# Kernel optimization log

Measured on AMD Instinct MI355X. Metric: run time of the kernel, lower is better.

Reference implementation:

```python
import jax, jax.numpy as jnp
import numpy as np

B, N, F = 1024, 256, 8
E = 1024
OUT = 128          # NNConv out-channels (hardcoded in module)
N_DIV = 64         # len(num_actions)
PER = 3            # actions per diverter
FEAT = N * OUT     # feature_size() = num_nodes * 128


def setup_inputs() -> dict:
    key = jax.random.key(0)
    ks = jax.random.split(key, 20)
    s = lambda *sh: 0.02
    return {
        "x": jax.random.normal(ks[0], (B, N, F), jnp.float32),
        "edge_index": jax.random.randint(ks[1], (2, E), 0, N, jnp.int64),
        # edge-MLP nn1: Linear(1,64) -> ReLU -> Linear(64, F*OUT)
        "w1": jax.random.normal(ks[2], (1, 64), jnp.float32) * 0.1,
        "b1": jnp.zeros((64,), jnp.float32),
        "w2": jax.random.normal(ks[3], (64, F * OUT), jnp.float32) * 0.02,
        "b2": jnp.zeros((F * OUT,), jnp.float32),
        # NNConv root weight + bias
        "root_w": jax.random.normal(ks[4], (F, OUT), jnp.float32) * 0.1,
        "conv_b": jnp.zeros((OUT,), jnp.float32),
        # dueling heads
        "adv_w": jax.random.normal(ks[5], (FEAT, N_DIV * PER), jnp.float32) * 0.005,
        "adv_b": jnp.zeros((N_DIV * PER,), jnp.float32),
        "v1w": jax.random.normal(ks[6], (FEAT, 64), jnp.float32) * 0.005,
        "v1b": jnp.zeros((64,), jnp.float32),
        "v2w": jax.random.normal(ks[7], (64, 64), jnp.float32) * 0.1,
        "v2b": jnp.zeros((64,), jnp.float32),
        "v3w": jax.random.normal(ks[8], (64, N_DIV), jnp.float32) * 0.1,
        "v3b": jnp.zeros((N_DIV,), jnp.float32),
    }


def reference(x, edge_index, w1, b1, w2, b2, root_w, conv_b,
              adv_w, adv_b, v1w, v1b, v2w, v2b, v3w, v3b):
    b, n, f = x.shape
    out_c = root_w.shape[1]
    n_div = v3w.shape[1]
    flat = x.reshape(b * n, f)                              # [B*N, F]
    e = edge_index.shape[1]
    # edge_attr = ones -> edge MLP produces per-edge weight matrix theta
    ea = jnp.ones((e, 1), x.dtype)
    h = jax.nn.relu(ea @ w1 + b1)
    theta = (h @ w2 + b2).reshape(e, f, out_c)              # [E, F, OUT]
    src, tgt = edge_index[0], edge_index[1]
    # gather source feats -> per-edge matmul -> scatter-add at targets
    msg = jnp.einsum('ef,efo->eo', flat[src], theta)        # [E, OUT]
    agg = jnp.zeros((b * n, out_c), x.dtype).at[tgt].add(msg)
    conv = agg + flat @ root_w + conv_b                      # NNConv root + bias
    feat = jax.nn.relu(conv).reshape(b, -1)                  # [B, N*OUT]
    adv = jax.nn.relu(feat @ adv_w + adv_b).reshape(b, n_div, -1)
    val = jax.nn.relu(feat @ v1w + v1b)
    val = jax.nn.relu(val @ v2w + v2b)
    val = val @ v3w + v3b                                    # [B, n_div]
    return val[..., None] + adv - adv.mean(-1, keepdims=True)
```

## Files before the change

kernel.cpp:

```cpp
#include <hip/hip_runtime.h>

#define Bsz 1024
#define Nn 256
#define Fdim 8
#define Eedge 1024
#define OUTC 128
#define CADV 192
#define CTOT 256
#define Ktot 32768
#define ASTR 40
#define XSTR 24

typedef __attribute__((ext_vector_type(8))) short short8;
typedef __attribute__((ext_vector_type(4))) float float4v;

static __device__ inline unsigned short f2bf(float f) {
  union { float f; unsigned u; } v; v.f = f;
  unsigned r = v.u + 0x7FFFu + ((v.u >> 16) & 1u);
  return (unsigned short)(r >> 16);
}
static __device__ inline float bf2f(unsigned short h) {
  union { unsigned u; float f; } v; v.u = ((unsigned)h) << 16;
  return v.f;
}
static __device__ inline uint4 pack8(const unsigned short* b) {
  uint4 v;
  v.x = (unsigned)b[0] | ((unsigned)b[1] << 16);
  v.y = (unsigned)b[2] | ((unsigned)b[3] << 16);
  v.z = (unsigned)b[4] | ((unsigned)b[5] << 16);
  v.w = (unsigned)b[6] | ((unsigned)b[7] << 16);
  return v;
}

__global__ __launch_bounds__(256) void prep_feat_kernel(
    const float* __restrict__ x, const int* __restrict__ ei,
    const float* __restrict__ w1, const float* __restrict__ b1,
    const float* __restrict__ w2, const float* __restrict__ b2,
    const float* __restrict__ rootw, const float* __restrict__ convb,
    const float* __restrict__ advw, const float* __restrict__ v1w,
    unsigned short* __restrict__ wt, unsigned short* __restrict__ feat0)
{
  __shared__ __align__(16) char smem[20480];
  int bid = blockIdx.x, t = threadIdx.x;

  if (bid < 16) {
    float* fs   = (float*)smem;
    float* h_s  = fs;
    float* rw_s = fs + 64;
    float* th_s = fs + 128;
    float* pt_s = fs + 192;
    float* S_s  = fs + 448;
    int*   flag = (int*)(fs + 2496);
    int obase = bid * 8;

    if (t < 64) {
      h_s[t]  = fmaxf(w1[t] + b1[t], 0.f);
      rw_s[t] = rootw[(t >> 3) * OUTC + obase + (t & 7)];
    }
    for (int i = t; i < Nn * Fdim; i += 256) S_s[i] = 0.f;
    if (t == 0) {
      int z = 0;
      for (int i = 1; i < 16; i += 2) z |= ei[i];
      *flag = (z == 0);
    }
    __syncthreads();
    int is64 = *flag;

    {
      int l = t & 63, g = t >> 6;
      int c = (l >> 3) * 128 + obase + (l & 7);
      float p = 0.f;
#pragma unroll
      for (int j = 0; j < 16; ++j)
        p += h_s[g * 16 + j] * w2[(size_t)(g * 16 + j) * 1024 + c];
      pt_s[t] = p;
    }
    int srcs[4], tgts[4];
#pragma unroll
    for (int q = 0; q < 4; ++q) {
      int e = t + q * 256;
      if (is64) { srcs[q] = ei[2 * e]; tgts[q] = ei[2 * (Eedge + e)]; }
      else      { srcs[q] = ei[e];     tgts[q] = ei[Eedge + e]; }
      srcs[q] &= 255; tgts[q] &= 255;
    }
    __syncthreads();
    if (t < 64) {
      int c = (t >> 3) * 128 + obase + (t & 7);
      th_s[t] = b2[c] + pt_s[t] + pt_s[t + 64] + pt_s[t + 128] + pt_s[t + 192];
    }
#pragma unroll
    for (int q = 0; q < 4; ++q) {
      const float* xp = x + srcs[q] * Fdim;
#pragma unroll
      for (int f = 0; f < Fdim; ++f)
        atomicAdd(&S_s[tgts[q] * Fdim + f], xp[f]);
    }
    __syncthreads();
    {
      int n = t;
      const float* xp = x + n * Fdim;
      float4 xa = *(const float4*)xp;
      float4 xb = *(const float4*)(xp + 4);
      float xv[8] = {xa.x, xa.y, xa.z, xa.w, xb.x, xb.y, xb.z, xb.w};
      float sv[8];
#pragma unroll
      for (int f = 0; f < 8; ++f) sv[f] = S_s[n * Fdim + f];
      unsigned short buf[8];
#pragma unroll
      for (int oi = 0; oi < 8; ++oi) {
        float z = convb[obase + oi];
#pragma unroll
        for (int f = 0; f < 8; ++f)
          z += xv[f] * rw_s[f * 8 + oi] + sv[f] * th_s[f * 8 + oi];
        buf[oi] = f2bf(fmaxf(z, 0.f));
      }
      *(uint4*)(feat0 + (size_t)n * OUTC + obase) = pack8(buf);
    }
  } else {
    unsigned short* st = (unsigned short*)smem;
    int kt = bid - 16, c = t;
    const float* src; int stride, col;
    if (c < CADV) { src = advw; stride = CADV; col = c; }
    else          { src = v1w;  stride = 64;   col = c - CADV; }
    float v[32];
#pragma unroll
    for (int i = 0; i < 32; ++i)
      v[i] = src[(size_t)(kt * 32 + i) * stride + col];
    unsigned short bv[32];
#pragma unroll
    for (int i = 0; i < 32; ++i) bv[i] = f2bf(v[i]);
#pragma unroll
    for (int p = 0; p < 4; ++p)
      *(uint4*)(st + c * ASTR + p * 8) = pack8(bv + p * 8);
    __syncthreads();
    uint4* dst = (uint4*)(wt + (size_t)kt * (CTOT * 32));
    for (int r = 0; r < 4; ++r) {
      int w = r * 256 + c;
      int wn = w >> 8, j = (w >> 6) & 3, ln = w & 63;
      int c2 = wn * 64 + j * 16 + (ln & 15);
      int ks = ln >> 4;
      dst[w] = *(const uint4*)(st + c2 * ASTR + ks * 8);
    }
  }
}

__global__ __launch_bounds__(512, 2) void gemm_mfma(
    const float* __restrict__ x, const unsigned short* __restrict__ wt,
    const float* __restrict__ rootw, const float* __restrict__ convb,
    const unsigned short* __restrict__ feat0, float* __restrict__ part,
    int iters, int ns)
{
  __shared__ short a_s[2][128 * ASTR];
  __shared__ short x_s[2][128 * XSTR];
  __shared__ short rw_s[128 * XSTR];
  __shared__ float convb_s[128];
  int t = threadIdx.x;
  int ch = blockIdx.x;
  int mb = blockIdx.y;
  int wave = t >> 6, lane = t & 63;
  int wm = wave >> 2, wn = wave & 3;
  int lm = lane & 15, lq = lane >> 4;

  float4v acc[4][4];
#pragma unroll
  for (int i = 0; i < 4; ++i)
#pragma unroll
    for (int j = 0; j < 4; ++j) acc[i][j] = (float4v)0.f;

  int kt0 = ch * iters;
  int iters4 = iters >> 2;
  int n0 = ch * iters4;
  int boff = wn * 256 + lane;

  if (t < 128) {
    float wv[8];
#pragma unroll
    for (int f = 0; f < 8; ++f) wv[f] = rootw[f * OUTC + t];
    unsigned short wh[8], wl[8];
#pragma unroll
    for (int f = 0; f < 8; ++f) {
      wh[f] = f2bf(wv[f]);
      wl[f] = f2bf(wv[f] - bf2f(wh[f]));
    }
    *(uint4*)(rw_s + t * XSTR)     = pack8(wh);
    *(uint4*)(rw_s + t * XSTR + 8) = pack8(wl);
    convb_s[t] = convb[t];
  }
  int xr = (t & 255) >> 1, xh = t & 1;
  const float* xgb = x + ((size_t)(mb * 128 + xr) * Nn) * Fdim + xh * 4;
  if (t < 256) {
    float4 xv = *(const float4*)(xgb + (size_t)n0 * Fdim);
    float xa[4] = {xv.x, xv.y, xv.z, xv.w};
    unsigned short hh[4], ll[4];
#pragma unroll
    for (int f = 0; f < 4; ++f) {
      hh[f] = f2bf(xa[f]);
      ll[f] = f2bf(xa[f] - bf2f(hh[f]));
    }
    uint2 dh, dl;
    dh.x = (unsigned)hh[0] | ((unsigned)hh[1] << 16);
    dh.y = (unsigned)hh[2] | ((unsigned)hh[3] << 16);
    dl.x = (unsigned)ll[0] | ((unsigned)ll[1] << 16);
    dl.y = (unsigned)ll[2] | ((unsigned)ll[3] << 16);
    *(uint2*)(x_s[0] + xr * XSTR + xh * 4)     = dh;
    *(uint2*)(x_s[0] + xr * XSTR + 8 + xh * 4) = dl;
  }
  __syncthreads();

  {
    int bloc = wave * 16 + lm;
    short8 xf = (short8)0;
    if (lq == 0 || lq == 2) xf = *(const short8*)(x_s[0] + bloc * XSTR);
    else if (lq == 1)       xf = *(const short8*)(x_s[0] + bloc * XSTR + 8);
#pragma unroll
    for (int tt = 0; tt < 2; ++tt) {
      int ot = tt;
      short8 wf = (short8)0;
      if (lq <= 1)      wf = *(const short8*)(rw_s + (ot * 16 + lm) * XSTR);
      else if (lq == 2) wf = *(const short8*)(rw_s + (ot * 16 + lm) * XSTR + 8);
      float4v c = __builtin_amdgcn_mfma_f32_16x16x32_bf16(wf, xf, (float4v)0.f, 0, 0, 0);
      int o0 = ot * 16 + lq * 4;
      float4 cb = *(const float4*)(convb_s + o0);
      unsigned d0 = (unsigned)f2bf(fmaxf(c[0] + cb.x, 0.f)) |
                    ((unsigned)f2bf(fmaxf(c[1] + cb.y, 0.f)) << 16);
      unsigned d1 = (unsigned)f2bf(fmaxf(c[2] + cb.z, 0.f)) |
                    ((unsigned)f2bf(fmaxf(c[3] + cb.w, 0.f)) << 16);
      if (mb == 0 && bloc == 0) {
        const unsigned* f0p = (const unsigned*)(feat0 + ((size_t)n0 * OUTC + o0));
        d0 = f0p[0]; d1 = f0p[1];
      }
      uint2 dd; dd.x = d0; dd.y = d1;
      *(uint2*)(a_s[0] + bloc * ASTR + tt * 16 + lq * 4) = dd;
    }
  }

  const uint4* gB = (const uint4*)wt;
  uint4 vb0, vb1, vb2, vb3;
  {
    const uint4* gq = gB + (size_t)kt0 * 1024 + boff;
    vb0 = gq[0]; vb1 = gq[64]; vb2 = gq[128]; vb3 = gq[192];
  }
  float4 xpf = {0.f, 0.f, 0.f, 0.f};

  for (int kk = 0; kk < iters; ++kk) {
    int g = kk & 3, grp = kk >> 2;
    if (g == 3 && grp + 1 < iters4 && t < 256) {
      float xa[4] = {xpf.x, xpf.y, xpf.z, xpf.w};
      unsigned short hh[4], ll[4];
#pragma unroll
      for (int f = 0; f < 4; ++f) {
        hh[f] = f2bf(xa[f]);
        ll[f] = f2bf(xa[f] - bf2f(hh[f]));
      }
      uint2 dh, dl;
      dh.x = (unsigned)hh[0] | ((unsigned)hh[1] << 16);
      dh.y = (unsigned)hh[2] | ((unsigned)hh[3] << 16);
      dl.x = (unsigned)ll[0] | ((unsigned)ll[1] << 16);
      dl.y = (unsigned)ll[2] | ((unsigned)ll[3] << 16);
      short* xd = x_s[(grp + 1) & 1];
      *(uint2*)(xd + xr * XSTR + xh * 4)     = dh;
      *(uint2*)(xd + xr * XSTR + 8 + xh * 4) = dl;
    }
    __syncthreads();

    uint4 vbn0, vbn1, vbn2, vbn3;
    bool pf = (kk + 1 < iters);
    if (pf) {
      const uint4* gq = gB + (size_t)(kt0 + kk + 1) * 1024 + boff;
      vbn0 = gq[0]; vbn1 = gq[64]; vbn2 = gq[128]; vbn3 = gq[192];
    }
    if (g == 0 && grp + 1 < iters4 && t < 256)
      xpf = *(const float4*)(xgb + (size_t)(n0 + grp + 1) * Fdim);

    short* ab = a_s[kk & 1];
    short8 aF[4];
#pragma unroll
    for (int i = 0; i < 4; ++i)
      aF[i] = *(const short8*)(ab + (wm * 64 + i * 16 + lm) * ASTR + lq * 8);
    {
      short8 bF;
      bF = *(short8*)&vb0;
#pragma unroll
      for (int i = 0; i < 4; ++i)
        acc[i][0] = __builtin_amdgcn_mfma_f32_16x16x32_bf16(bF, aF[i], acc[i][0], 0, 0, 0);
      bF = *(short8*)&vb1;
#pragma unroll
      for (int i = 0; i < 4; ++i)
        acc[i][1] = __builtin_amdgcn_mfma_f32_16x16x32_bf16(bF, aF[i], acc[i][1], 0, 0, 0);
      bF = *(short8*)&vb2;
#pragma unroll
      for (int i = 0; i < 4; ++i)
        acc[i][2] = __builtin_amdgcn_mfma_f32_16x16x32_bf16(bF, aF[i], acc[i][2], 0, 0, 0);
      bF = *(short8*)&vb3;
#pragma unroll
      for (int i = 0; i < 4; ++i)
        acc[i][3] = __builtin_amdgcn_mfma_f32_16x16x32_bf16(bF, aF[i], acc[i][3], 0, 0, 0);
    }

    if (pf) {
      int kn = kk + 1;
      int g2 = kn & 3, grp2 = kn >> 2;
      const short* xs = x_s[grp2 & 1];
      int node2 = n0 + grp2;
      short* ad = a_s[kn & 1];
      int bloc = wave * 16 + lm;
      short8 xf = (short8)0;
      if (lq == 0 || lq == 2) xf = *(const short8*)(xs + bloc * XSTR);
      else if (lq == 1)       xf = *(const short8*)(xs + bloc * XSTR + 8);
#pragma unroll
      for (int tt = 0; tt < 2; ++tt) {
        int ot = g2 * 2 + tt;
        short8 wf = (short8)0;
        if (lq <= 1)      wf = *(const short8*)(rw_s + (ot * 16 + lm) * XSTR);
        else if (lq == 2) wf = *(const short8*)(rw_s + (ot * 16 + lm) * XSTR + 8);
        float4v c = __builtin_amdgcn_mfma_f32_16x16x32_bf16(wf, xf, (float4v)0.f, 0, 0, 0);
        int o0 = ot * 16 + lq * 4;
        float4 cb = *(const float4*)(convb_s + o0);
        unsigned d0 = (unsigned)f2bf(fmaxf(c[0] + cb.x, 0.f)) |
                      ((unsigned)f2bf(fmaxf(c[1] + cb.y, 0.f)) << 16);
        unsigned d1 = (unsigned)f2bf(fmaxf(c[2] + cb.z, 0.f)) |
                      ((unsigned)f2bf(fmaxf(c[3] + cb.w, 0.f)) << 16);
        if (mb == 0 && bloc == 0) {
          const unsigned* f0p = (const unsigned*)(feat0 + ((size_t)node2 * OUTC + o0));
          d0 = f0p[0]; d1 = f0p[1];
        }
        uint2 dd; dd.x = d0; dd.y = d1;
        *(uint2*)(ad + bloc * ASTR + tt * 16 + lq * 4) = dd;
      }
      vb0 = vbn0; vb1 = vbn1; vb2 = vbn2; vb3 = vbn3;
    }
  }

  float* pb = part + ((size_t)(mb * 128) * ns + ch) * CTOT;
#pragma unroll
  for (int i = 0; i < 4; ++i) {
    int m = wm * 64 + i * 16 + lm;
#pragma unroll
    for (int j = 0; j < 4; ++j) {
      int c = wn * 64 + j * 16 + lq * 4;
      *(float4v*)(pb + (size_t)m * ns * CTOT + c) = acc[i][j];
    }
  }
}

__global__ __launch_bounds__(256) void final_kernel(
    const float* __restrict__ part, int ns,
    const float* __restrict__ advb, const float* __restrict__ v1b,
    const float* __restrict__ v2w, const float* __restrict__ v2b,
    const float* __restrict__ v3w, const float* __restrict__ v3b,
    float* __restrict__ out)
{
  __shared__ float adv_s[CADV];
  __shared__ float v1_s[64];
  __shared__ float val2_s[64];
  __shared__ float val3_s[64];
  int b = blockIdx.x, t = threadIdx.x;
  float s = 0.f;
  const float* p = part + (size_t)b * ns * CTOT + t;
  for (int i = 0; i < ns; ++i) s += p[(size_t)i * CTOT];
  if (t < CADV) adv_s[t] = fmaxf(s + advb[t], 0.f);
  else          v1_s[t - CADV] = fmaxf(s + v1b[t - CADV], 0.f);
  __syncthreads();
  if (t < 64) {
    float a = v2b[t];
#pragma unroll
    for (int i = 0; i < 64; ++i) a += v1_s[i] * v2w[i * 64 + t];
    val2_s[t] = fmaxf(a, 0.f);
  }
  __syncthreads();
  if (t < 64) {
    float a = v3b[t];
#pragma unroll
    for (int j = 0; j < 64; ++j) a += val2_s[j] * v3w[j * 64 + t];
    val3_s[t] = a;
  }
  __syncthreads();
  if (t < CADV) {
    int d = t / 3;
    float mean = (adv_s[d * 3] + adv_s[d * 3 + 1] + adv_s[d * 3 + 2]) * (1.f / 3.f);
    out[(size_t)b * CADV + t] = val3_s[d] + adv_s[t] - mean;
  }
}

extern "C" void kernel_launch(void* const* d_in, const int* in_sizes, int n_in,
                              void* d_out, int out_size, void* d_ws, size_t ws_size,
                              hipStream_t stream)
{
  (void)in_sizes; (void)n_in; (void)out_size;
  const float* x     = (const float*)d_in[0];
  const int*   ei    = (const int*)d_in[1];
  const float* w1    = (const float*)d_in[2];
  const float* b1    = (const float*)d_in[3];
  const float* w2    = (const float*)d_in[4];
  const float* b2    = (const float*)d_in[5];
  const float* rootw = (const float*)d_in[6];
  const float* convb = (const float*)d_in[7];
  const float* advw  = (const float*)d_in[8];
  const float* advb  = (const float*)d_in[9];
  const float* v1w   = (const float*)d_in[10];
  const float* v1b   = (const float*)d_in[11];
  const float* v2w   = (const float*)d_in[12];
  const float* v2b   = (const float*)d_in[13];
  const float* v3w   = (const float*)d_in[14];
  const float* v3b   = (const float*)d_in[15];
  float* out = (float*)d_out;

  const size_t f0B = 131072;
  const size_t wtB = (size_t)Ktot * CTOT * 2;

  int NS = 64;
  while (NS > 8 && f0B + wtB + (size_t)NS * Bsz * CTOT * 4 > ws_size)
    NS >>= 1;

  unsigned short* feat0 = (unsigned short*)d_ws;
  unsigned short* wtp   = (unsigned short*)((char*)d_ws + f0B);
  float* part = (float*)((char*)d_ws + f0B + wtB);

  prep_feat_kernel<<<1040, 256, 0, stream>>>(x, ei, w1, b1, w2, b2, rootw,
                                             convb, advw, v1w, wtp, feat0);
  gemm_mfma<<<dim3(NS, 8), 512, 0, stream>>>(x, wtp, rootw, convb, feat0, part,
                                             1024 / NS, NS);
  final_kernel<<<Bsz, 256, 0, stream>>>(part, NS, advb, v1b, v2w, v2b, v3w, v3b, out);
}
```

Measured before the change: 185.5 us.

## Halve GEMM M-tile to 64 rows, double grid, drop B register prefetch

Shrinks the per-block batch tile in the MFMA GEMM from 128 to 64 rows, doubles the grid's M dimension to 16 and raises the launch-bounds occupancy hint from 2 to 4 blocks. Each wave now builds a single 16-column slice of the root-conv A tile instead of two. The one-iteration-ahead register prefetch of the weight fragments is removed, so B is loaded at the top of each iteration. The goal is more concurrent blocks and fewer registers to hide latency, at the price of reading the bf16 weight stream twice as many times and losing the explicit B prefetch.

```diff
diff --git a/kernel.cpp b/kernel.cpp
--- a/kernel.cpp
+++ b/kernel.cpp
@@ -144,14 +144,14 @@
   }
 }
 
-__global__ __launch_bounds__(512, 2) void gemm_mfma(
+__global__ __launch_bounds__(512, 4) void gemm_mfma(
     const float* __restrict__ x, const unsigned short* __restrict__ wt,
     const float* __restrict__ rootw, const float* __restrict__ convb,
     const unsigned short* __restrict__ feat0, float* __restrict__ part,
     int iters, int ns)
 {
-  __shared__ short a_s[2][128 * ASTR];
-  __shared__ short x_s[2][128 * XSTR];
+  __shared__ short a_s[2][64 * ASTR];
+  __shared__ short x_s[2][64 * XSTR];
   __shared__ short rw_s[128 * XSTR];
   __shared__ float convb_s[128];
   int t = threadIdx.x;
@@ -161,9 +161,9 @@
   int wm = wave >> 2, wn = wave & 3;
   int lm = lane & 15, lq = lane >> 4;
 
-  float4v acc[4][4];
-#pragma unroll
-  for (int i = 0; i < 4; ++i)
+  float4v acc[2][4];
+#pragma unroll
+  for (int i = 0; i < 2; ++i)
 #pragma unroll
     for (int j = 0; j < 4; ++j) acc[i][j] = (float4v)0.f;
 
@@ -171,6 +171,8 @@
   int iters4 = iters >> 2;
   int n0 = ch * iters4;
   int boff = wn * 256 + lane;
+  int bloc2 = (wave & 3) * 16 + lm;
+  int ttg = wave >> 2;
 
   if (t < 128) {
     float wv[8];
@@ -186,9 +188,9 @@
     *(uint4*)(rw_s + t * XSTR + 8) = pack8(wl);
     convb_s[t] = convb[t];
   }
-  int xr = (t & 255) >> 1, xh = t & 1;
-  const float* xgb = x + ((size_t)(mb * 128 + xr) * Nn) * Fdim + xh * 4;
-  if (t < 256) {
+  int xr = (t & 127) >> 1, xh = t & 1;
+  const float* xgb = x + ((size_t)(mb * 64 + xr) * Nn) * Fdim + xh * 4;
+  if (t < 128) {
     float4 xv = *(const float4*)(xgb + (size_t)n0 * Fdim);
     float xa[4] = {xv.x, xv.y, xv.z, xv.w};
     unsigned short hh[4], ll[4];
@@ -208,43 +210,34 @@
   __syncthreads();
 
   {
-    int bloc = wave * 16 + lm;
     short8 xf = (short8)0;
-    if (lq == 0 || lq == 2) xf = *(const short8*)(x_s[0] + bloc * XSTR);
-    else if (lq == 1)       xf = *(const short8*)(x_s[0] + bloc * XSTR + 8);
-#pragma unroll
-    for (int tt = 0; tt < 2; ++tt) {
-      int ot = tt;
-      short8 wf = (short8)0;
-      if (lq <= 1)      wf = *(const short8*)(rw_s + (ot * 16 + lm) * XSTR);
-      else if (lq == 2) wf = *(const short8*)(rw_s + (ot * 16 + lm) * XSTR + 8);
-      float4v c = __builtin_amdgcn_mfma_f32_16x16x32_bf16(wf, xf, (float4v)0.f, 0, 0, 0);
-      int o0 = ot * 16 + lq * 4;
-      float4 cb = *(const float4*)(convb_s + o0);
-      unsigned d0 = (unsigned)f2bf(fmaxf(c[0] + cb.x, 0.f)) |
-                    ((unsigned)f2bf(fmaxf(c[1] + cb.y, 0.f)) << 16);
-      unsigned d1 = (unsigned)f2bf(fmaxf(c[2] + cb.z, 0.f)) |
-                    ((unsigned)f2bf(fmaxf(c[3] + cb.w, 0.f)) << 16);
-      if (mb == 0 && bloc == 0) {
-        const unsigned* f0p = (const unsigned*)(feat0 + ((size_t)n0 * OUTC + o0));
-        d0 = f0p[0]; d1 = f0p[1];
-      }
-      uint2 dd; dd.x = d0; dd.y = d1;
-      *(uint2*)(a_s[0] + bloc * ASTR + tt * 16 + lq * 4) = dd;
-    }
+    if (lq == 0 || lq == 2) xf = *(const short8*)(x_s[0] + bloc2 * XSTR);
+    else if (lq == 1)       xf = *(const short8*)(x_s[0] + bloc2 * XSTR + 8);
+    int ot = ttg;
+    short8 wf = (short8)0;
+    if (lq <= 1)      wf = *(const short8*)(rw_s + (ot * 16 + lm) * XSTR);
+    else if (lq == 2) wf = *(const short8*)(rw_s + (ot * 16 + lm) * XSTR + 8);
+    float4v c = __builtin_amdgcn_mfma_f32_16x16x32_bf16(wf, xf, (float4v)0.f, 0, 0, 0);
+    int o0 = ot * 16 + lq * 4;
+    float4 cb = *(const float4*)(convb_s + o0);
+    unsigned d0 = (unsigned)f2bf(fmaxf(c[0] + cb.x, 0.f)) |
+                  ((unsigned)f2bf(fmaxf(c[1] + cb.y, 0.f)) << 16);
+    unsigned d1 = (unsigned)f2bf(fmaxf(c[2] + cb.z, 0.f)) |
+                  ((unsigned)f2bf(fmaxf(c[3] + cb.w, 0.f)) << 16);
+    if (mb == 0 && bloc2 == 0) {
+      const unsigned* f0p = (const unsigned*)(feat0 + ((size_t)n0 * OUTC + o0));
+      d0 = f0p[0]; d1 = f0p[1];
+    }
+    uint2 dd; dd.x = d0; dd.y = d1;
+    *(uint2*)(a_s[0] + bloc2 * ASTR + ttg * 16 + lq * 4) = dd;
   }
 
   const uint4* gB = (const uint4*)wt;
-  uint4 vb0, vb1, vb2, vb3;
-  {
-    const uint4* gq = gB + (size_t)kt0 * 1024 + boff;
-    vb0 = gq[0]; vb1 = gq[64]; vb2 = gq[128]; vb3 = gq[192];
-  }
   float4 xpf = {0.f, 0.f, 0.f, 0.f};
 
   for (int kk = 0; kk < iters; ++kk) {
     int g = kk & 3, grp = kk >> 2;
-    if (g == 3 && grp + 1 < iters4 && t < 256) {
+    if (g == 3 && grp + 1 < iters4 && t < 128) {
       float xa[4] = {xpf.x, xpf.y, xpf.z, xpf.w};
       unsigned short hh[4], ll[4];
 #pragma unroll
@@ -263,78 +256,69 @@
     }
     __syncthreads();
 
-    uint4 vbn0, vbn1, vbn2, vbn3;
-    bool pf = (kk + 1 < iters);
-    if (pf) {
-      const uint4* gq = gB + (size_t)(kt0 + kk + 1) * 1024 + boff;
-      vbn0 = gq[0]; vbn1 = gq[64]; vbn2 = gq[128]; vbn3 = gq[192];
-    }
-    if (g == 0 && grp + 1 < iters4 && t < 256)
+    const uint4* gq = gB + (size_t)(kt0 + kk) * 1024 + boff;
+    uint4 vb0 = gq[0], vb1 = gq[64], vb2 = gq[128], vb3 = gq[192];
+    if (g == 0 && grp + 1 < iters4 && t < 128)
       xpf = *(const float4*)(xgb + (size_t)(n0 + grp + 1) * Fdim);
 
     short* ab = a_s[kk & 1];
-    short8 aF[4];
-#pragma unroll
-    for (int i = 0; i < 4; ++i)
-      aF[i] = *(const short8*)(ab + (wm * 64 + i * 16 + lm) * ASTR + lq * 8);
+    short8 aF[2];
+#pragma unroll
+    for (int i = 0; i < 2; ++i)
+      aF[i] = *(const short8*)(ab + (wm * 32 + i * 16 + lm) * ASTR + lq * 8);
     {
       short8 bF;
       bF = *(short8*)&vb0;
 #pragma unroll
-      for (int i = 0; i < 4; ++i)
+      for (int i = 0; i < 2; ++i)
         acc[i][0] = __builtin_amdgcn_mfma_f32_16x16x32_bf16(bF, aF[i], acc[i][0], 0, 0, 0);
       bF = *(short8*)&vb1;
 #pragma unroll
-      for (int i = 0; i < 4; ++i)
+      for (int i = 0; i < 2; ++i)
         acc[i][1] = __builtin_amdgcn_mfma_f32_16x16x32_bf16(bF, aF[i], acc[i][1], 0, 0, 0);
       bF = *(short8*)&vb2;
 #pragma unroll
-      for (int i = 0; i < 4; ++i)
+      for (int i = 0; i < 2; ++i)
         acc[i][2] = __builtin_amdgcn_mfma_f32_16x16x32_bf16(bF, aF[i], acc[i][2], 0, 0, 0);
       bF = *(short8*)&vb3;
 #pragma unroll
-      for (int i = 0; i < 4; ++i)
+      for (int i = 0; i < 2; ++i)
         acc[i][3] = __builtin_amdgcn_mfma_f32_16x16x32_bf16(bF, aF[i], acc[i][3], 0, 0, 0);
     }
 
-    if (pf) {
+    if (kk + 1 < iters) {
       int kn = kk + 1;
       int g2 = kn & 3, grp2 = kn >> 2;
       const short* xs = x_s[grp2 & 1];
       int node2 = n0 + grp2;
       short* ad = a_s[kn & 1];
-      int bloc = wave * 16 + lm;
       short8 xf = (short8)0;
-      if (lq == 0 || lq == 2) xf = *(const short8*)(xs + bloc * XSTR);
-      else if (lq == 1)       xf = *(const short8*)(xs + bloc * XSTR + 8);
-#pragma unroll
-      for (int tt = 0; tt < 2; ++tt) {
-        int ot = g2 * 2 + tt;
-        short8 wf = (short8)0;
-        if (lq <= 1)      wf = *(const short8*)(rw_s + (ot * 16 + lm) * XSTR);
-        else if (lq == 2) wf = *(const short8*)(rw_s + (ot * 16 + lm) * XSTR + 8);
-        float4v c = __builtin_amdgcn_mfma_f32_16x16x32_bf16(wf, xf, (float4v)0.f, 0, 0, 0);
-        int o0 = ot * 16 + lq * 4;
-        float4 cb = *(const float4*)(convb_s + o0);
-        unsigned d0 = (unsigned)f2bf(fmaxf(c[0] + cb.x, 0.f)) |
-                      ((unsigned)f2bf(fmaxf(c[1] + cb.y, 0.f)) << 16);
-        unsigned d1 = (unsigned)f2bf(fmaxf(c[2] + cb.z, 0.f)) |
-                      ((unsigned)f2bf(fmaxf(c[3] + cb.w, 0.f)) << 16);
-        if (mb == 0 && bloc == 0) {
-          const unsigned* f0p = (const unsigned*)(feat0 + ((size_t)node2 * OUTC + o0));
-          d0 = f0p[0]; d1 = f0p[1];
-        }
-        uint2 dd; dd.x = d0; dd.y = d1;
-        *(uint2*)(ad + bloc * ASTR + tt * 16 + lq * 4) = dd;
+      if (lq == 0 || lq == 2) xf = *(const short8*)(xs + bloc2 * XSTR);
+      else if (lq == 1)       xf = *(const short8*)(xs + bloc2 * XSTR + 8);
+      int ot = g2 * 2 + ttg;
+      short8 wf = (short8)0;
+      if (lq <= 1)      wf = *(const short8*)(rw_s + (ot * 16 + lm) * XSTR);
+      else if (lq == 2) wf = *(const short8*)(rw_s + (ot * 16 + lm) * XSTR + 8);
+      float4v c = __builtin_amdgcn_mfma_f32_16x16x32_bf16(wf, xf, (float4v)0.f, 0, 0, 0);
+      int o0 = ot * 16 + lq * 4;
+      float4 cb = *(const float4*)(convb_s + o0);
+      unsigned d0 = (unsigned)f2bf(fmaxf(c[0] + cb.x, 0.f)) |
+                    ((unsigned)f2bf(fmaxf(c[1] + cb.y, 0.f)) << 16);
+      unsigned d1 = (unsigned)f2bf(fmaxf(c[2] + cb.z, 0.f)) |
+                    ((unsigned)f2bf(fmaxf(c[3] + cb.w, 0.f)) << 16);
+      if (mb == 0 && bloc2 == 0) {
+        const unsigned* f0p = (const unsigned*)(feat0 + ((size_t)node2 * OUTC + o0));
+        d0 = f0p[0]; d1 = f0p[1];
       }
-      vb0 = vbn0; vb1 = vbn1; vb2 = vbn2; vb3 = vbn3;
-    }
-  }
-
-  float* pb = part + ((size_t)(mb * 128) * ns + ch) * CTOT;
-#pragma unroll
-  for (int i = 0; i < 4; ++i) {
-    int m = wm * 64 + i * 16 + lm;
+      uint2 dd; dd.x = d0; dd.y = d1;
+      *(uint2*)(ad + bloc2 * ASTR + ttg * 16 + lq * 4) = dd;
+    }
+  }
+
+  float* pb = part + ((size_t)(mb * 64) * ns + ch) * CTOT;
+#pragma unroll
+  for (int i = 0; i < 2; ++i) {
+    int m = wm * 32 + i * 16 + lm;
 #pragma unroll
     for (int j = 0; j < 4; ++j) {
       int c = wn * 64 + j * 16 + lq * 4;
@@ -418,7 +402,7 @@
 
   prep_feat_kernel<<<1040, 256, 0, stream>>>(x, ei, w1, b1, w2, b2, rootw,
                                              convb, advw, v1w, wtp, feat0);
-  gemm_mfma<<<dim3(NS, 8), 512, 0, stream>>>(x, wtp, rootw, convb, feat0, part,
-                                             1024 / NS, NS);
+  gemm_mfma<<<dim3(NS, 16), 512, 0, stream>>>(x, wtp, rootw, convb, feat0, part,
+                                              1024 / NS, NS);
   final_kernel<<<Bsz, 256, 0, stream>>>(part, NS, advb, v1b, v2w, v2b, v3w, v3b, out);
 }
```

Result: faster. 178.9 us (-3.6%).
